# Performance work log

Hardware: AMD Instinct MI355X
Metric: run time of the kernel (lower is better)

## Reference

```python
import jax, jax.numpy as jnp
import numpy as np

B, T, N, F_IN = 8, 12, 20000, 2
H, HORIZON, K = 64, 12, 2
E = 320000


def setup_inputs() -> dict:
    key = jax.random.key(0)
    ks = jax.random.split(key, 12)
    s = 0.05
    return dict(
        x=jax.random.normal(ks[0], (B, T, N, F_IN), jnp.float32),
        edge_index=jax.random.randint(ks[1], (2, E), 0, N),
        edge_weight=jax.random.uniform(ks[2], (E,), jnp.float32),
        enc_w=jax.random.normal(ks[3], (F_IN, H), jnp.float32) * s,
        enc_b=jnp.zeros((H,), jnp.float32),
        node_emb=jax.random.normal(ks[4], (N, H), jnp.float32) * s,
        w_ih=jax.random.normal(ks[5], (3 * H, H), jnp.float32) * s,
        w_hh=jax.random.normal(ks[6], (3 * H, H), jnp.float32) * s,
        b_ih=jnp.zeros((3 * H,), jnp.float32),
        b_hh=jnp.zeros((3 * H,), jnp.float32),
        filt_w=jax.random.normal(ks[7], (H * (2 * K + 1), H), jnp.float32) * s,
        filt_b=jnp.zeros((H,), jnp.float32),
        dec_w=jax.random.normal(ks[8], (H, F_IN * HORIZON), jnp.float32) * s,
        dec_b=jnp.zeros((F_IN * HORIZON,), jnp.float32),
    )


def _gru_last(x_seq, w_ih, w_hh, b_ih, b_hh):
    # x_seq: [BN, T, H] -> last hidden state [BN, H] (torch GRU gate math)
    bn = x_seq.shape[0]
    h0 = jnp.zeros((bn, H), x_seq.dtype)
    # precompute input-side gates: [T, BN, 3H]
    xg = jnp.swapaxes(jnp.einsum('bth,gh->btg', x_seq, w_ih) + b_ih, 0, 1)

    def step(h, xg_t):
        hg = h @ w_hh.T + b_hh
        xr, xz, xn = jnp.split(xg_t, 3, axis=-1)
        hr, hz, hn = jnp.split(hg, 3, axis=-1)
        r = jax.nn.sigmoid(xr + hr)
        z = jax.nn.sigmoid(xz + hz)
        n = jnp.tanh(xn + r * hn)
        return (1.0 - z) * n + z * h, None

    h_last, _ = jax.lax.scan(step, h0, xg)
    return h_last


def _norm_weights(w, idx):
    # normalize edge weights by in-degree of aggregation index (tsl normalize)
    deg = jax.ops.segment_sum(w, idx, num_segments=N)
    inv = jnp.where(deg > 0, 1.0 / deg, 0.0)
    return w * inv[idx]


def _propagate(h, src, tgt, w):
    # h: [B, N, H]; message x_j * w aggregated (sum) at target
    msg = h[:, src, :] * w[None, :, None]           # [B, E, H]
    return jnp.zeros_like(h).at[:, tgt, :].add(msg)


def reference(x, edge_index, edge_weight, enc_w, enc_b, node_emb,
              w_ih, w_hh, b_ih, b_hh, filt_w, filt_b, dec_w, dec_b):
    b, t, n, _ = x.shape
    # linear encode + node embeddings
    x_emb = x @ enc_w + enc_b + node_emb[None, None]          # [B, T, N, H]
    # per-node GRU over time
    x_rnn = jnp.transpose(x_emb, (0, 2, 1, 3)).reshape(b * n, t, H)
    h = _gru_last(x_rnn, w_ih, w_hh, b_ih, b_hh).reshape(b, n, H)
    # diffusion graph conv: root + k hops forward + k hops backward
    src, tgt = edge_index[0], edge_index[1]
    w_fwd = _norm_weights(edge_weight, tgt)
    w_bwd = _norm_weights(edge_weight, src)
    outs = [h]
    for s_idx, t_idx, w in ((src, tgt, w_fwd), (tgt, src, w_bwd)):
        hs = h
        for _ in range(K):
            hs = _propagate(hs, s_idx, t_idx, w)
            outs.append(hs)
    z = jnp.concatenate(outs, axis=-1) @ filt_w + filt_b      # [B, N, H]
    # decode and rearrange 'b n (t f) -> b t n f'
    x_out = z @ dec_w + dec_b                                 # [B, N, HORIZON*F_IN]
    x_hor = x_out.reshape(b, n, HORIZON, F_IN)
    return jnp.transpose(x_hor, (0, 2, 1, 3))                 # [B, HORIZON, N, F_IN]
```

## Files before the change

### kernel.cpp

```cpp
#include <hip/hip_runtime.h>

#define NN 20000
#define NE 320000
#define NB 8
#define NT 12

typedef unsigned int u32;
typedef short bf16x8 __attribute__((ext_vector_type(8)));
typedef float f32x4 __attribute__((ext_vector_type(4)));

union U8 { u32 u[4]; bf16x8 v; };

__device__ __forceinline__ float bcast(float v, int k) {
  return __int_as_float(__builtin_amdgcn_readlane(__float_as_int(v), k));
}
__device__ __forceinline__ u32 cvt_pk_bf16(float a, float b) {
  u32 r;
  asm("v_cvt_pk_bf16_f32 %0, %1, %2" : "=v"(r) : "v"(a), "v"(b));
  return r;
}
__device__ __forceinline__ float rcpf(float x) {
  float r;
  asm("v_rcp_f32 %0, %1" : "=v"(r) : "v"(x));
  return r;
}
__device__ __forceinline__ unsigned short f2bf(float f) {
  u32 u = __float_as_uint(f);
  u32 r = (u + 0x7FFFu + ((u >> 16) & 1u)) >> 16;
  return (unsigned short)r;
}
__device__ __forceinline__ float bf2f(unsigned short s) {
  return __uint_as_float(((u32)s) << 16);
}

__global__ void deg_kernel(const int* __restrict__ ei, const float* __restrict__ ew,
                           float* __restrict__ wsum_f, float* __restrict__ wsum_b,
                           int* __restrict__ cnt_f, int* __restrict__ cnt_b) {
  int e = blockIdx.x * 256 + threadIdx.x;
  if (e >= NE) return;
  int s = ei[e], t = ei[NE + e];
  float wv = ew[e];
  atomicAdd(&wsum_f[t], wv);
  atomicAdd(&cnt_f[t], 1);
  atomicAdd(&wsum_b[s], wv);
  atomicAdd(&cnt_b[s], 1);
}

__global__ __launch_bounds__(1024) void scan_kernel(
    const int* __restrict__ cnt_f, const int* __restrict__ cnt_b,
    int* __restrict__ rp_f, int* __restrict__ rp_b,
    int* __restrict__ cur_f, int* __restrict__ cur_b) {
  __shared__ int sm[1024];
  const int tid = threadIdx.x;
  for (int pass = 0; pass < 2; ++pass) {
    const int* cnt = pass ? cnt_b : cnt_f;
    int* rp  = pass ? rp_b  : rp_f;
    int* cur = pass ? cur_b : cur_f;
    const int base = tid * 20;
    int4 c4[5];
    int s = 0;
    if (base < NN) {
      const int4* cp = (const int4*)(cnt + base);
#pragma unroll
      for (int j = 0; j < 5; j++) c4[j] = cp[j];
#pragma unroll
      for (int j = 0; j < 5; j++) s += c4[j].x + c4[j].y + c4[j].z + c4[j].w;
    }
    __syncthreads();
    sm[tid] = s;
    __syncthreads();
    for (int off = 1; off < 1024; off <<= 1) {
      int v = (tid >= off) ? sm[tid - off] : 0;
      __syncthreads();
      sm[tid] += v;
      __syncthreads();
    }
    if (base < NN) {
      int run = sm[tid] - s;
      int4* rp4  = (int4*)(rp + base);
      int4* cur4 = (int4*)(cur + base);
#pragma unroll
      for (int j = 0; j < 5; j++) {
        int4 o;
        o.x = run; run += c4[j].x;
        o.y = run; run += c4[j].y;
        o.z = run; run += c4[j].z;
        o.w = run; run += c4[j].w;
        rp4[j] = o;
        cur4[j] = o;
      }
    }
    if (tid == 1023) rp[NN] = sm[1023];
  }
}

__global__ void fill_kernel(const int* __restrict__ ei, const float* __restrict__ ew,
                            const float* __restrict__ wsum_f, const float* __restrict__ wsum_b,
                            int* __restrict__ cur_f, int* __restrict__ cur_b,
                            int* __restrict__ col_f, float* __restrict__ wn_f,
                            int* __restrict__ col_b, float* __restrict__ wn_b) {
  int e = blockIdx.x * 256 + threadIdx.x;
  if (e >= NE) return;
  int s = ei[e], t = ei[NE + e];
  float wv = ew[e];
  int slot = atomicAdd(&cur_f[t], 1);
  float w1 = wsum_f[t];
  col_f[slot] = s;
  wn_f[slot] = (w1 > 0.f) ? wv / w1 : 0.f;
  slot = atomicAdd(&cur_b[s], 1);
  float w2 = wsum_b[s];
  col_b[slot] = t;
  wn_b[slot] = (w2 > 0.f) ? wv / w2 : 0.f;
}

#define NBLK_NB 313
__global__ __launch_bounds__(512) void nb_kernel(
    const float* __restrict__ node_emb, const float* __restrict__ enc_b,
    const float* __restrict__ w_ih, const float* __restrict__ b_ih,
    const float* __restrict__ enc_w, const float* __restrict__ b_hh,
    const float* __restrict__ filt_w, const float* __restrict__ filt_b,
    const float* __restrict__ dec_w, const float* __restrict__ dec_b,
    float* __restrict__ nbq, float* __restrict__ W2,
    float* __restrict__ Wcat, float* __restrict__ cbv) {
  const int tid = threadIdx.x;
  if (blockIdx.x >= NBLK_NB) {
    int idx = (blockIdx.x - NBLK_NB) * 512 + tid;
    if (idx < 64 * 128) {
      int k = idx >> 7, j = idx & 127;
      float acc = 0.f;
      if (j < 120) {
        int wi = j / 24, jj = j - wi * 24;
        for (int c = 0; c < 64; c++)
          acc += filt_w[(wi * 64 + k) * 64 + c] * dec_w[c * 24 + jj];
      }
      Wcat[idx] = acc;
    } else if (idx < 64 * 128 + 24) {
      int jj = idx - 64 * 128;
      float acc = dec_b[jj];
      for (int c = 0; c < 64; c++) acc += filt_b[c] * dec_w[c * 24 + jj];
      cbv[jj] = acc;
    }
    return;
  }
  __shared__ float w3[64 * 64 * 4];
  for (int idx = tid; idx < 192 * 64; idx += 512) {
    int row = idx >> 6, k = idx & 63;
    w3[((k << 6) + (row & 63)) * 4 + (row >> 6)] = w_ih[idx];
  }
  __syncthreads();
  const int lane = tid & 63, wave = tid >> 6;
  const float4* w3v = (const float4*)w3;
  const float eb = enc_b[lane];
  const float bir = b_ih[lane], biz = b_ih[64 + lane], bin_ = b_ih[128 + lane];
  const float bhr = b_hh[lane], bhz = b_hh[64 + lane];
#pragma unroll 1
  for (int pass = 0; pass < 8; ++pass) {
    const int n = blockIdx.x * 64 + pass * 8 + wave;
    if (n >= NN) break;
    float ne = node_emb[n * 64 + lane] + eb;
    float ar = bir, az = biz, an = bin_;
#pragma unroll 16
    for (int k = 0; k < 64; k++) {
      float4 w = w3v[(k << 6) + lane];
      float nk = bcast(ne, k);
      ar = fmaf(w.x, nk, ar);
      az = fmaf(w.y, nk, az);
      an = fmaf(w.z, nk, an);
    }
    nbq[(((lane >> 2)) * NN + n) * 4 + (lane & 3)]      = ar + bhr;
    nbq[((16 + (lane >> 2)) * NN + n) * 4 + (lane & 3)] = az + bhz;
    nbq[((32 + (lane >> 2)) * NN + n) * 4 + (lane & 3)] = an;
  }
  if (blockIdx.x == 0 && tid < 384) {
    int f = tid / 192, g = tid - f * 192;
    float acc = 0.f;
    for (int k2 = 0; k2 < 64; k2++) acc += enc_w[f * 64 + k2] * w_ih[g * 64 + k2];
    W2[f * 192 + g] = acc;
  }
}

#define MFMA(acc, a, b) acc = __builtin_amdgcn_mfma_f32_16x16x32_bf16((a), (b), acc, 0, 0, 0)
#define BP(addr, reg) __builtin_amdgcn_ds_bpermute((addr), (int)(reg))

__global__ __launch_bounds__(256, 3) void gru_kernel(
    const float* __restrict__ x, const float* __restrict__ nbq,
    const float* __restrict__ W2, const float* __restrict__ b_hh,
    const float* __restrict__ w_hh, const float* __restrict__ Wcat,
    const float* __restrict__ cbv,
    float* __restrict__ G0, float* __restrict__ G1f, float* __restrict__ G2f,
    float* __restrict__ G1b, float* __restrict__ G2b) {
  __shared__ u32 lds[12288];
  const int tid = threadIdx.x;

  for (int idx = tid; idx < 6144; idx += 256) {
    int tile = idx >> 9, ks = (idx >> 8) & 1, ln = (idx >> 2) & 63, r = idx & 3;
    int gate = tile * 16 + (ln & 15);
    int k2 = ks * 32 + ((ln >> 4) & 3) * 8 + r * 2;
    float w0 = w_hh[gate * 64 + k2];
    float w1 = w_hh[gate * 64 + k2 + 1];
    unsigned short h0 = f2bf(w0), h1 = f2bf(w1);
    unsigned short l0 = f2bf(w0 - bf2f(h0)), l1 = f2bf(w1 - bf2f(h1));
    lds[idx]        = (u32)h0 | ((u32)h1 << 16);
    lds[6144 + idx] = (u32)l0 | ((u32)l1 << 16);
  }
  __syncthreads();

  const int lane = tid & 63, wave = tid >> 6;
  const int g = lane >> 4, sl = lane & 15;
  const int seq = blockIdx.x * 64 + wave * 16 + sl;
  const int bb = seq / NN;
  const int node = seq - bb * NN;
  const int addrA = (((g & 1) * 32) + sl) * 4;
  const int addrB = addrA + 64;
  const bool fbHi = (g >= 2);

#define LDW(tile, ks, part) (*(const bf16x8*)(lds + (part) * 6144 + (((tile) * 2 + (ks)) << 8) + (lane << 2)))

#define BLD(hb, lb, fo) { \
    int a_, b_; \
    a_ = BP(addrA, hiP[fo]); b_ = BP(addrA, hiP[(fo) + 1]); hb.u[0] = fbHi ? b_ : a_; \
    a_ = BP(addrA, hiQ[fo]); b_ = BP(addrA, hiQ[(fo) + 1]); hb.u[1] = fbHi ? b_ : a_; \
    a_ = BP(addrB, hiP[fo]); b_ = BP(addrB, hiP[(fo) + 1]); hb.u[2] = fbHi ? b_ : a_; \
    a_ = BP(addrB, hiQ[fo]); b_ = BP(addrB, hiQ[(fo) + 1]); hb.u[3] = fbHi ? b_ : a_; \
    a_ = BP(addrA, loP[fo]); b_ = BP(addrA, loP[(fo) + 1]); lb.u[0] = fbHi ? b_ : a_; \
    a_ = BP(addrA, loQ[fo]); b_ = BP(addrA, loQ[(fo) + 1]); lb.u[1] = fbHi ? b_ : a_; \
    a_ = BP(addrB, loP[fo]); b_ = BP(addrB, loP[(fo) + 1]); lb.u[2] = fbHi ? b_ : a_; \
    a_ = BP(addrB, loQ[fo]); b_ = BP(addrB, loQ[(fo) + 1]); lb.u[3] = fbHi ? b_ : a_; \
  }

  u32 w2h[12], w2l[12];
#pragma unroll
  for (int tl = 0; tl < 12; tl++) {
    float w0 = W2[tl * 16 + sl], w1 = W2[192 + tl * 16 + sl];
    u32 ph = cvt_pk_bf16(w0, w1);
    float lo0 = w0 - __uint_as_float(ph << 16);
    float lo1 = w1 - __uint_as_float(ph & 0xffff0000u);
    u32 pl = cvt_pk_bf16(lo0, lo1);
    w2h[tl] = (lane < 16) ? ph : 0u;
    w2l[tl] = (lane < 16) ? pl : 0u;
  }

  f32x4 nbA[4], nbB[4], nbC[4], bhnv[4];
#pragma unroll
  for (int fb = 0; fb < 4; fb++) {
    nbA[fb]  = *(const f32x4*)(nbq + ((size_t)(fb * 4 + g) * NN + node) * 4);
    nbB[fb]  = *(const f32x4*)(nbq + ((size_t)(16 + fb * 4 + g) * NN + node) * 4);
    nbC[fb]  = *(const f32x4*)(nbq + ((size_t)(32 + fb * 4 + g) * NN + node) * 4);
    bhnv[fb] = *(const f32x4*)(b_hh + 128 + fb * 16 + g * 4);
  }

  f32x4 hreg[4];
#pragma unroll
  for (int fb = 0; fb < 4; fb++) hreg[fb] = (f32x4){0.f, 0.f, 0.f, 0.f};

  u32 hiP[4], hiQ[4], loP[4], loQ[4];

  const float* xptr = x + ((size_t)(bb * NT) * NN + node) * 2;

  U8 hb0, hb1, lb0, lb1;

  float2 xv = *(const float2*)(xptr);

#pragma unroll 1
  for (int t = 0; t < NT; t++) {
    float2 xvn;
    if (t + 1 < NT) xvn = *(const float2*)(xptr + (size_t)(t + 1) * (NN * 2));
    u32 xhw = cvt_pk_bf16(xv.x, xv.y);
    float xl0 = xv.x - __uint_as_float(xhw << 16);
    float xl1 = xv.y - __uint_as_float(xhw & 0xffff0000u);
    u32 xlw = cvt_pk_bf16(xl0, xl1);
    U8 xB;
    xB.u[0] = xhw; xB.u[1] = xlw; xB.u[2] = xhw; xB.u[3] = 0u;

    if (t) { BLD(hb0, lb0, 0); BLD(hb1, lb1, 2); }

#pragma unroll
    for (int fb = 0; fb < 4; fb++) {
      f32x4 aR = nbA[fb], aZ = nbB[fb], aXN = nbC[fb], aHN = bhnv[fb];
      if (t) {
        bf16x8 Ah0 = LDW(fb, 0, 0), Al0 = LDW(fb, 0, 1);
        bf16x8 Ah1 = LDW(fb, 1, 0), Al1 = LDW(fb, 1, 1);
        MFMA(aR, Ah0, hb0.v); MFMA(aR, Ah0, lb0.v); MFMA(aR, Al0, hb0.v);
        MFMA(aR, Ah1, hb1.v); MFMA(aR, Ah1, lb1.v); MFMA(aR, Al1, hb1.v);
        bf16x8 Bh0 = LDW(4 + fb, 0, 0), Bl0 = LDW(4 + fb, 0, 1);
        bf16x8 Bh1 = LDW(4 + fb, 1, 0), Bl1 = LDW(4 + fb, 1, 1);
        MFMA(aZ, Bh0, hb0.v); MFMA(aZ, Bh0, lb0.v); MFMA(aZ, Bl0, hb0.v);
        MFMA(aZ, Bh1, hb1.v); MFMA(aZ, Bh1, lb1.v); MFMA(aZ, Bl1, hb1.v);
        bf16x8 Ch0 = LDW(8 + fb, 0, 0), Cl0 = LDW(8 + fb, 0, 1);
        bf16x8 Ch1 = LDW(8 + fb, 1, 0), Cl1 = LDW(8 + fb, 1, 1);
        MFMA(aHN, Ch0, hb0.v); MFMA(aHN, Ch0, lb0.v); MFMA(aHN, Cl0, hb0.v);
        MFMA(aHN, Ch1, hb1.v); MFMA(aHN, Ch1, lb1.v); MFMA(aHN, Cl1, hb1.v);
      }
      U8 aW;
      aW.u[0] = w2h[fb];     aW.u[1] = w2h[fb];     aW.u[2] = w2l[fb];     aW.u[3] = 0u;
      MFMA(aR, aW.v, xB.v);
      aW.u[0] = w2h[4 + fb]; aW.u[1] = w2h[4 + fb]; aW.u[2] = w2l[4 + fb];
      MFMA(aZ, aW.v, xB.v);
      aW.u[0] = w2h[8 + fb]; aW.u[1] = w2h[8 + fb]; aW.u[2] = w2l[8 + fb];
      MFMA(aXN, aW.v, xB.v);

      float hv[4];
#pragma unroll
      for (int r = 0; r < 4; r++) {
        float rr = rcpf(1.f + __expf(-aR[r]));
        float zz = rcpf(1.f + __expf(-aZ[r]));
        float nv = fmaf(rr, aHN[r], aXN[r]);
        float th = fmaf(-2.f, rcpf(1.f + __expf(2.f * nv)), 1.f);
        float h2 = fmaf(zz, hreg[fb][r] - th, th);
        hreg[fb][r] = h2;
        hv[r] = h2;
      }
      u32 hA = cvt_pk_bf16(hv[0], hv[1]);
      u32 hB = cvt_pk_bf16(hv[2], hv[3]);
      float l0 = hv[0] - __uint_as_float(hA << 16);
      float l1 = hv[1] - __uint_as_float(hA & 0xffff0000u);
      float l2 = hv[2] - __uint_as_float(hB << 16);
      float l3 = hv[3] - __uint_as_float(hB & 0xffff0000u);
      hiP[fb] = hA;
      hiQ[fb] = hB;
      loP[fb] = cvt_pk_bf16(l0, l1);
      loQ[fb] = cvt_pk_bf16(l2, l3);
    }
    xv = xvn;
  }

  __syncthreads();
  for (int idx = tid; idx < 4096; idx += 256) {
    int tile = idx >> 9, ks = (idx >> 8) & 1, ln = (idx >> 2) & 63, r = idx & 3;
    int j = tile * 16 + (ln & 15);
    int k2 = ks * 32 + ((ln >> 4) & 3) * 8 + r * 2;
    float w0 = Wcat[k2 * 128 + j];
    float w1 = Wcat[(k2 + 1) * 128 + j];
    unsigned short h0 = f2bf(w0), h1 = f2bf(w1);
    unsigned short l0 = f2bf(w0 - bf2f(h0)), l1 = f2bf(w1 - bf2f(h1));
    lds[idx]        = (u32)h0 | ((u32)h1 << 16);
    lds[4096 + idx] = (u32)l0 | ((u32)l1 << 16);
  }
  __syncthreads();
  BLD(hb0, lb0, 0); BLD(hb1, lb1, 2);

#define LDC(tile, ks, part) (*(const bf16x8*)(lds + (part) * 4096 + (((tile) * 2 + (ks)) << 8) + (lane << 2)))
#pragma unroll
  for (int tile = 0; tile < 8; tile++) {
    f32x4 acc = (f32x4){0.f, 0.f, 0.f, 0.f};
    bf16x8 Ah0 = LDC(tile, 0, 0), Al0 = LDC(tile, 0, 1);
    MFMA(acc, Ah0, hb0.v); MFMA(acc, Ah0, lb0.v); MFMA(acc, Al0, hb0.v);
    bf16x8 Ah1 = LDC(tile, 1, 0), Al1 = LDC(tile, 1, 1);
    MFMA(acc, Ah1, hb1.v); MFMA(acc, Ah1, lb1.v); MFMA(acc, Al1, hb1.v);
#pragma unroll
    for (int r = 0; r < 4; r++) {
      int j = tile * 16 + g * 4 + r;
      if (j < 120) {
        int wi = j / 24, jj = j - wi * 24;
        float val = acc[r];
        if (wi == 0) val += cbv[jj];
        float* gb = (wi == 0) ? G0 : (wi == 1) ? G1f : (wi == 2) ? G2f : (wi == 3) ? G1b : G2b;
        gb[((size_t)node * NB + bb) * 24 + jj] = val;
      }
    }
  }
}

__global__ __launch_bounds__(256) void hop1_kernel(
    float* __restrict__ G1f, const float* __restrict__ G2f,
    float* __restrict__ G1b, const float* __restrict__ G2b,
    const int* __restrict__ rp_f, const int* __restrict__ col_f, const float* __restrict__ wn_f,
    const int* __restrict__ rp_b, const int* __restrict__ col_b, const float* __restrict__ wn_b) {
  const int wv = threadIdx.x >> 6;
  const int lane = threadIdx.x & 63;
  const int task = blockIdx.x * 4 + wv;
  const int fwd = task < NN;
  const int n = fwd ? task : task - NN;
  const int* rp  = fwd ? rp_f : rp_b;
  const int* col = fwd ? col_f : col_b;
  const float* wn = fwd ? wn_f : wn_b;
  const float4* src = (const float4*)(fwd ? G2f : G2b);
  float4* dst = (float4*)(fwd ? G1f : G1b);
  const int e0 = rp[n], e1 = rp[n + 1];
  if (lane >= 48) return;
  float4 acc = {0.f, 0.f, 0.f, 0.f};
  for (int e = e0; e < e1; ++e) {
    const int c = col[e];
    const float w = wn[e];
    float4 v = src[(size_t)c * 48 + lane];
    acc.x = fmaf(w, v.x, acc.x);
    acc.y = fmaf(w, v.y, acc.y);
    acc.z = fmaf(w, v.z, acc.z);
    acc.w = fmaf(w, v.w, acc.w);
  }
  float4 d = dst[(size_t)n * 48 + lane];
  d.x += acc.x; d.y += acc.y; d.z += acc.z; d.w += acc.w;
  dst[(size_t)n * 48 + lane] = d;
}

__global__ __launch_bounds__(256) void hop2_kernel(
    float* __restrict__ G0, const float* __restrict__ G1f, const float* __restrict__ G1b,
    const int* __restrict__ rp_f, const int* __restrict__ col_f, const float* __restrict__ wn_f,
    const int* __restrict__ rp_b, const int* __restrict__ col_b, const float* __restrict__ wn_b) {
  const int wv = threadIdx.x >> 6;
  const int lane = threadIdx.x & 63;
  const int n = blockIdx.x * 4 + wv;
  if (lane >= 48) return;
  const float4* s1 = (const float4*)G1f;
  const float4* s2 = (const float4*)G1b;
  float4* dst = (float4*)G0;
  float4 acc = dst[(size_t)n * 48 + lane];
  int e0 = rp_f[n], e1 = rp_f[n + 1];
  for (int e = e0; e < e1; ++e) {
    const int c = col_f[e];
    const float w = wn_f[e];
    float4 v = s1[(size_t)c * 48 + lane];
    acc.x = fmaf(w, v.x, acc.x);
    acc.y = fmaf(w, v.y, acc.y);
    acc.z = fmaf(w, v.z, acc.z);
    acc.w = fmaf(w, v.w, acc.w);
  }
  e0 = rp_b[n]; e1 = rp_b[n + 1];
  for (int e = e0; e < e1; ++e) {
    const int c = col_b[e];
    const float w = wn_b[e];
    float4 v = s2[(size_t)c * 48 + lane];
    acc.x = fmaf(w, v.x, acc.x);
    acc.y = fmaf(w, v.y, acc.y);
    acc.z = fmaf(w, v.z, acc.z);
    acc.w = fmaf(w, v.w, acc.w);
  }
  dst[(size_t)n * 48 + lane] = acc;
}

__global__ __launch_bounds__(256) void reorder_kernel(const float* __restrict__ G0,
                                                      float* __restrict__ out) {
  __shared__ float tile[32 * 193];
  const int n0 = blockIdx.x * 32;
  const int tid = threadIdx.x;
  for (int idx = tid; idx < 6144; idx += 256) {
    int i = idx / 192, r = idx - i * 192;
    tile[i * 193 + r] = G0[(size_t)n0 * 192 + idx];
  }
  __syncthreads();
  for (int idx = tid; idx < 6144; idx += 256) {
    int b = idx / 768;
    int rem = idx - b * 768;
    int t = rem >> 6;
    int rem2 = rem & 63;
    int i = rem2 >> 1, f = rem2 & 1;
    out[(((size_t)b * NT + t) * NN + n0 + i) * 2 + f] = tile[i * 193 + b * 24 + t * 2 + f];
  }
}

extern "C" void kernel_launch(void* const* d_in, const int* in_sizes, int n_in,
                              void* d_out, int out_size, void* d_ws, size_t ws_size,
                              hipStream_t stream) {
  const float* x        = (const float*)d_in[0];
  const int*   ei       = (const int*)d_in[1];
  const float* ew       = (const float*)d_in[2];
  const float* enc_w    = (const float*)d_in[3];
  const float* enc_b    = (const float*)d_in[4];
  const float* node_emb = (const float*)d_in[5];
  const float* w_ih     = (const float*)d_in[6];
  const float* w_hh     = (const float*)d_in[7];
  const float* b_ih     = (const float*)d_in[8];
  const float* b_hh     = (const float*)d_in[9];
  const float* filt_w   = (const float*)d_in[10];
  const float* filt_b   = (const float*)d_in[11];
  const float* dec_w    = (const float*)d_in[12];
  const float* dec_b    = (const float*)d_in[13];
  float* out = (float*)d_out;

  char* p = (char*)d_ws;
  auto alloc = [&](size_t bytes) {
    char* r = p;
    p += (bytes + 255) & ~(size_t)255;
    return r;
  };
  const size_t BN24 = (size_t)NB * NN * 24;
  float* G0   = (float*)alloc(BN24 * 4);
  float* G1f  = (float*)alloc(BN24 * 4);
  float* G2f  = (float*)alloc(BN24 * 4);
  float* G1b  = (float*)alloc(BN24 * 4);
  float* G2b  = (float*)alloc(BN24 * 4);
  float* nbq  = (float*)alloc((size_t)NN * 192 * 4);
  int* rp_f   = (int*)alloc((NN + 1) * 4);
  int* rp_b   = (int*)alloc((NN + 1) * 4);
  char* zreg  = alloc(4 * NN * 4);
  float* wsum_f = (float*)zreg;
  float* wsum_b = wsum_f + NN;
  int*   cnt_f  = (int*)(wsum_b + NN);
  int*   cnt_b  = cnt_f + NN;
  int* cur_f  = (int*)alloc(NN * 4);
  int* cur_b  = (int*)alloc(NN * 4);
  int* col_f  = (int*)alloc((size_t)NE * 4);
  float* wn_f = (float*)alloc((size_t)NE * 4);
  int* col_b  = (int*)alloc((size_t)NE * 4);
  float* wn_b = (float*)alloc((size_t)NE * 4);
  float* Wcat = (float*)alloc(64 * 128 * 4);
  float* cbv  = (float*)alloc(32 * 4);
  float* W2   = (float*)alloc(384 * 4);

  hipMemsetAsync(zreg, 0, 4 * NN * 4, stream);
  deg_kernel<<<(NE + 255) / 256, 256, 0, stream>>>(ei, ew, wsum_f, wsum_b, cnt_f, cnt_b);
  scan_kernel<<<1, 1024, 0, stream>>>(cnt_f, cnt_b, rp_f, rp_b, cur_f, cur_b);
  fill_kernel<<<(NE + 255) / 256, 256, 0, stream>>>(ei, ew, wsum_f, wsum_b, cur_f, cur_b,
                                                    col_f, wn_f, col_b, wn_b);
  nb_kernel<<<NBLK_NB + 17, 512, 0, stream>>>(node_emb, enc_b, w_ih, b_ih, enc_w, b_hh,
                                              filt_w, filt_b, dec_w, dec_b,
                                              nbq, W2, Wcat, cbv);
  gru_kernel<<<(NB * NN) / 64, 256, 0, stream>>>(x, nbq, W2, b_hh, w_hh, Wcat, cbv,
                                                 G0, G1f, G2f, G1b, G2b);
  hop1_kernel<<<2 * NN / 4, 256, 0, stream>>>(G1f, G2f, G1b, G2b,
                                              rp_f, col_f, wn_f, rp_b, col_b, wn_b);
  hop2_kernel<<<NN / 4, 256, 0, stream>>>(G0, G1f, G1b,
                                          rp_f, col_f, wn_f, rp_b, col_b, wn_b);
  reorder_kernel<<<NN / 32, 256, 0, stream>>>(G0, out);
}
```

Baseline: 585.2 us.

## Remap GRU sequences to node-major blocks and unroll time loop by three

```diff
diff --git a/kernel.cpp b/kernel.cpp
--- a/kernel.cpp
+++ b/kernel.cpp
@@ -207,9 +207,8 @@
 
   const int lane = tid & 63, wave = tid >> 6;
   const int g = lane >> 4, sl = lane & 15;
-  const int seq = blockIdx.x * 64 + wave * 16 + sl;
-  const int bb = seq / NN;
-  const int node = seq - bb * NN;
+  const int node = blockIdx.x * 8 + (sl & 7);
+  const int bb = wave * 2 + (sl >> 3);
   const int addrA = (((g & 1) * 32) + sl) * 4;
   const int addrB = addrA + 64;
   const bool fbHi = (g >= 2);
@@ -259,12 +258,7 @@
 
   U8 hb0, hb1, lb0, lb1;
 
-  float2 xv = *(const float2*)(xptr);
-
-#pragma unroll 1
-  for (int t = 0; t < NT; t++) {
-    float2 xvn;
-    if (t + 1 < NT) xvn = *(const float2*)(xptr + (size_t)(t + 1) * (NN * 2));
+  auto body = [&](float2 xv, bool doH) {
     u32 xhw = cvt_pk_bf16(xv.x, xv.y);
     float xl0 = xv.x - __uint_as_float(xhw << 16);
     float xl1 = xv.y - __uint_as_float(xhw & 0xffff0000u);
@@ -272,12 +266,12 @@
     U8 xB;
     xB.u[0] = xhw; xB.u[1] = xlw; xB.u[2] = xhw; xB.u[3] = 0u;
 
-    if (t) { BLD(hb0, lb0, 0); BLD(hb1, lb1, 2); }
+    if (doH) { BLD(hb0, lb0, 0); BLD(hb1, lb1, 2); }
 
 #pragma unroll
     for (int fb = 0; fb < 4; fb++) {
       f32x4 aR = nbA[fb], aZ = nbB[fb], aXN = nbC[fb], aHN = bhnv[fb];
-      if (t) {
+      if (doH) {
         bf16x8 Ah0 = LDW(fb, 0, 0), Al0 = LDW(fb, 0, 1);
         bf16x8 Ah1 = LDW(fb, 1, 0), Al1 = LDW(fb, 1, 1);
         MFMA(aR, Ah0, hb0.v); MFMA(aR, Ah0, lb0.v); MFMA(aR, Al0, hb0.v);
@@ -321,7 +315,23 @@
       loP[fb] = cvt_pk_bf16(l0, l1);
       loQ[fb] = cvt_pk_bf16(l2, l3);
     }
-    xv = xvn;
+  };
+
+  float2 xc0 = *(const float2*)(xptr);
+  float2 xc1 = *(const float2*)(xptr + (size_t)(NN * 2));
+  float2 xc2 = *(const float2*)(xptr + (size_t)2 * (NN * 2));
+#pragma unroll 1
+  for (int tb = 0; tb < 4; tb++) {
+    float2 xn0, xn1, xn2;
+    if (tb < 3) {
+      xn0 = *(const float2*)(xptr + (size_t)(3 * tb + 3) * (NN * 2));
+      xn1 = *(const float2*)(xptr + (size_t)(3 * tb + 4) * (NN * 2));
+      xn2 = *(const float2*)(xptr + (size_t)(3 * tb + 5) * (NN * 2));
+    }
+    body(xc0, tb != 0);
+    body(xc1, true);
+    body(xc2, true);
+    xc0 = xn0; xc1 = xn1; xc2 = xn2;
   }
 
   __syncthreads();
@@ -505,8 +515,8 @@
   nb_kernel<<<NBLK_NB + 17, 512, 0, stream>>>(node_emb, enc_b, w_ih, b_ih, enc_w, b_hh,
                                               filt_w, filt_b, dec_w, dec_b,
                                               nbq, W2, Wcat, cbv);
-  gru_kernel<<<(NB * NN) / 64, 256, 0, stream>>>(x, nbq, W2, b_hh, w_hh, Wcat, cbv,
-                                                 G0, G1f, G2f, G1b, G2b);
+  gru_kernel<<<NN / 8, 256, 0, stream>>>(x, nbq, W2, b_hh, w_hh, Wcat, cbv,
+                                         G0, G1f, G2f, G1b, G2b);
   hop1_kernel<<<2 * NN / 4, 256, 0, stream>>>(G1f, G2f, G1b, G2b,
                                               rp_f, col_f, wn_f, rp_b, col_b, wn_b);
   hop2_kernel<<<NN / 4, 256, 0, stream>>>(G0, G1f, G1b,
```

Result: slower. 1.240 ms (+111.9%).

## Precompute bf16 hi/lo weight splits in a prep kernel; halve GRU LDS footprint

Applied to the files above, without the earlier changes.

```diff
diff --git a/kernel.cpp b/kernel.cpp
--- a/kernel.cpp
+++ b/kernel.cpp
@@ -179,30 +179,49 @@
   }
 }
 
-#define MFMA(acc, a, b) acc = __builtin_amdgcn_mfma_f32_16x16x32_bf16((a), (b), acc, 0, 0, 0)
-#define BP(addr, reg) __builtin_amdgcn_ds_bpermute((addr), (int)(reg))
-
-__global__ __launch_bounds__(256, 3) void gru_kernel(
-    const float* __restrict__ x, const float* __restrict__ nbq,
-    const float* __restrict__ W2, const float* __restrict__ b_hh,
+__global__ __launch_bounds__(256) void prep_kernel(
     const float* __restrict__ w_hh, const float* __restrict__ Wcat,
-    const float* __restrict__ cbv,
-    float* __restrict__ G0, float* __restrict__ G1f, float* __restrict__ G2f,
-    float* __restrict__ G1b, float* __restrict__ G2b) {
-  __shared__ u32 lds[12288];
-  const int tid = threadIdx.x;
-
-  for (int idx = tid; idx < 6144; idx += 256) {
+    u32* __restrict__ whhHi, u32* __restrict__ whhLo,
+    u32* __restrict__ wcatHi, u32* __restrict__ wcatLo) {
+  int idx = blockIdx.x * 256 + threadIdx.x;
+  if (idx < 6144) {
     int tile = idx >> 9, ks = (idx >> 8) & 1, ln = (idx >> 2) & 63, r = idx & 3;
     int gate = tile * 16 + (ln & 15);
     int k2 = ks * 32 + ((ln >> 4) & 3) * 8 + r * 2;
     float w0 = w_hh[gate * 64 + k2];
     float w1 = w_hh[gate * 64 + k2 + 1];
     unsigned short h0 = f2bf(w0), h1 = f2bf(w1);
-    unsigned short l0 = f2bf(w0 - bf2f(h0)), l1 = f2bf(w1 - bf2f(h1));
-    lds[idx]        = (u32)h0 | ((u32)h1 << 16);
-    lds[6144 + idx] = (u32)l0 | ((u32)l1 << 16);
-  }
+    whhHi[idx] = (u32)h0 | ((u32)h1 << 16);
+    whhLo[idx] = (u32)f2bf(w0 - bf2f(h0)) | ((u32)f2bf(w1 - bf2f(h1)) << 16);
+  } else if (idx < 6144 + 4096) {
+    int e = idx - 6144;
+    int tile = e >> 9, ks = (e >> 8) & 1, ln = (e >> 2) & 63, r = e & 3;
+    int j = tile * 16 + (ln & 15);
+    int k2 = ks * 32 + ((ln >> 4) & 3) * 8 + r * 2;
+    float w0 = Wcat[k2 * 128 + j];
+    float w1 = Wcat[(k2 + 1) * 128 + j];
+    unsigned short h0 = f2bf(w0), h1 = f2bf(w1);
+    wcatHi[e] = (u32)h0 | ((u32)h1 << 16);
+    wcatLo[e] = (u32)f2bf(w0 - bf2f(h0)) | ((u32)f2bf(w1 - bf2f(h1)) << 16);
+  }
+}
+
+#define MFMA(acc, a, b) acc = __builtin_amdgcn_mfma_f32_16x16x32_bf16((a), (b), acc, 0, 0, 0)
+#define BP(addr, reg) __builtin_amdgcn_ds_bpermute((addr), (int)(reg))
+
+__global__ __launch_bounds__(256, 4) void gru_kernel(
+    const float* __restrict__ x, const float* __restrict__ nbq,
+    const float* __restrict__ W2, const float* __restrict__ b_hh,
+    const u32* __restrict__ whhHi, const u32* __restrict__ whhLo,
+    const u32* __restrict__ wcatHi, const u32* __restrict__ wcatLo,
+    const float* __restrict__ cbv,
+    float* __restrict__ G0, float* __restrict__ G1f, float* __restrict__ G2f,
+    float* __restrict__ G1b, float* __restrict__ G2b) {
+  __shared__ __align__(16) u32 lds[6144];
+  const int tid = threadIdx.x;
+
+  for (int i = tid; i < 1536; i += 256)
+    ((uint4*)lds)[i] = ((const uint4*)whhHi)[i];
   __syncthreads();
 
   const int lane = tid & 63, wave = tid >> 6;
@@ -214,7 +233,8 @@
   const int addrB = addrA + 64;
   const bool fbHi = (g >= 2);
 
-#define LDW(tile, ks, part) (*(const bf16x8*)(lds + (part) * 6144 + (((tile) * 2 + (ks)) << 8) + (lane << 2)))
+#define LDH(tile, ks) (*(const bf16x8*)(lds + (((tile) * 2 + (ks)) << 8) + (lane << 2)))
+#define LDL(tile, ks) (*(const bf16x8*)(whhLo + (((tile) * 2 + (ks)) << 8) + (lane << 2)))
 
 #define BLD(hb, lb, fo) { \
     int a_, b_; \
@@ -278,16 +298,16 @@
     for (int fb = 0; fb < 4; fb++) {
       f32x4 aR = nbA[fb], aZ = nbB[fb], aXN = nbC[fb], aHN = bhnv[fb];
       if (t) {
-        bf16x8 Ah0 = LDW(fb, 0, 0), Al0 = LDW(fb, 0, 1);
-        bf16x8 Ah1 = LDW(fb, 1, 0), Al1 = LDW(fb, 1, 1);
+        bf16x8 Ah0 = LDH(fb, 0), Al0 = LDL(fb, 0);
+        bf16x8 Ah1 = LDH(fb, 1), Al1 = LDL(fb, 1);
         MFMA(aR, Ah0, hb0.v); MFMA(aR, Ah0, lb0.v); MFMA(aR, Al0, hb0.v);
         MFMA(aR, Ah1, hb1.v); MFMA(aR, Ah1, lb1.v); MFMA(aR, Al1, hb1.v);
-        bf16x8 Bh0 = LDW(4 + fb, 0, 0), Bl0 = LDW(4 + fb, 0, 1);
-        bf16x8 Bh1 = LDW(4 + fb, 1, 0), Bl1 = LDW(4 + fb, 1, 1);
+        bf16x8 Bh0 = LDH(4 + fb, 0), Bl0 = LDL(4 + fb, 0);
+        bf16x8 Bh1 = LDH(4 + fb, 1), Bl1 = LDL(4 + fb, 1);
         MFMA(aZ, Bh0, hb0.v); MFMA(aZ, Bh0, lb0.v); MFMA(aZ, Bl0, hb0.v);
         MFMA(aZ, Bh1, hb1.v); MFMA(aZ, Bh1, lb1.v); MFMA(aZ, Bl1, hb1.v);
-        bf16x8 Ch0 = LDW(8 + fb, 0, 0), Cl0 = LDW(8 + fb, 0, 1);
-        bf16x8 Ch1 = LDW(8 + fb, 1, 0), Cl1 = LDW(8 + fb, 1, 1);
+        bf16x8 Ch0 = LDH(8 + fb, 0), Cl0 = LDL(8 + fb, 0);
+        bf16x8 Ch1 = LDH(8 + fb, 1), Cl1 = LDL(8 + fb, 1);
         MFMA(aHN, Ch0, hb0.v); MFMA(aHN, Ch0, lb0.v); MFMA(aHN, Cl0, hb0.v);
         MFMA(aHN, Ch1, hb1.v); MFMA(aHN, Ch1, lb1.v); MFMA(aHN, Cl1, hb1.v);
       }
@@ -325,27 +345,19 @@
   }
 
   __syncthreads();
-  for (int idx = tid; idx < 4096; idx += 256) {
-    int tile = idx >> 9, ks = (idx >> 8) & 1, ln = (idx >> 2) & 63, r = idx & 3;
-    int j = tile * 16 + (ln & 15);
-    int k2 = ks * 32 + ((ln >> 4) & 3) * 8 + r * 2;
-    float w0 = Wcat[k2 * 128 + j];
-    float w1 = Wcat[(k2 + 1) * 128 + j];
-    unsigned short h0 = f2bf(w0), h1 = f2bf(w1);
-    unsigned short l0 = f2bf(w0 - bf2f(h0)), l1 = f2bf(w1 - bf2f(h1));
-    lds[idx]        = (u32)h0 | ((u32)h1 << 16);
-    lds[4096 + idx] = (u32)l0 | ((u32)l1 << 16);
-  }
+  for (int i = tid; i < 1024; i += 256)
+    ((uint4*)lds)[i] = ((const uint4*)wcatHi)[i];
   __syncthreads();
   BLD(hb0, lb0, 0); BLD(hb1, lb1, 2);
 
-#define LDC(tile, ks, part) (*(const bf16x8*)(lds + (part) * 4096 + (((tile) * 2 + (ks)) << 8) + (lane << 2)))
+#define LCH(tile, ks) (*(const bf16x8*)(lds + (((tile) * 2 + (ks)) << 8) + (lane << 2)))
+#define LCL(tile, ks) (*(const bf16x8*)(wcatLo + (((tile) * 2 + (ks)) << 8) + (lane << 2)))
 #pragma unroll
   for (int tile = 0; tile < 8; tile++) {
     f32x4 acc = (f32x4){0.f, 0.f, 0.f, 0.f};
-    bf16x8 Ah0 = LDC(tile, 0, 0), Al0 = LDC(tile, 0, 1);
+    bf16x8 Ah0 = LCH(tile, 0), Al0 = LCL(tile, 0);
     MFMA(acc, Ah0, hb0.v); MFMA(acc, Ah0, lb0.v); MFMA(acc, Al0, hb0.v);
-    bf16x8 Ah1 = LDC(tile, 1, 0), Al1 = LDC(tile, 1, 1);
+    bf16x8 Ah1 = LCH(tile, 1), Al1 = LCL(tile, 1);
     MFMA(acc, Ah1, hb1.v); MFMA(acc, Ah1, lb1.v); MFMA(acc, Al1, hb1.v);
 #pragma unroll
     for (int r = 0; r < 4; r++) {
@@ -496,6 +508,10 @@
   float* Wcat = (float*)alloc(64 * 128 * 4);
   float* cbv  = (float*)alloc(32 * 4);
   float* W2   = (float*)alloc(384 * 4);
+  u32* whhHi  = (u32*)alloc(6144 * 4);
+  u32* whhLo  = (u32*)alloc(6144 * 4);
+  u32* wcatHi = (u32*)alloc(4096 * 4);
+  u32* wcatLo = (u32*)alloc(4096 * 4);
 
   hipMemsetAsync(zreg, 0, 4 * NN * 4, stream);
   deg_kernel<<<(NE + 255) / 256, 256, 0, stream>>>(ei, ew, wsum_f, wsum_b, cnt_f, cnt_b);
@@ -505,7 +521,9 @@
   nb_kernel<<<NBLK_NB + 17, 512, 0, stream>>>(node_emb, enc_b, w_ih, b_ih, enc_w, b_hh,
                                               filt_w, filt_b, dec_w, dec_b,
                                               nbq, W2, Wcat, cbv);
-  gru_kernel<<<(NB * NN) / 64, 256, 0, stream>>>(x, nbq, W2, b_hh, w_hh, Wcat, cbv,
+  prep_kernel<<<40, 256, 0, stream>>>(w_hh, Wcat, whhHi, whhLo, wcatHi, wcatLo);
+  gru_kernel<<<(NB * NN) / 64, 256, 0, stream>>>(x, nbq, W2, b_hh,
+                                                 whhHi, whhLo, wcatHi, wcatLo, cbv,
                                                  G0, G1f, G2f, G1b, G2b);
   hop1_kernel<<<2 * NN / 4, 256, 0, stream>>>(G1f, G2f, G1b, G2b,
                                               rp_f, col_f, wn_f, rp_b, col_b, wn_b);
```

New measurement: 1.030 ms. +76.0%, slower.
